# Kernel tuning notes

Measured on AMD Instinct MI355X. Metric: run time of the kernel, lower is better.

The kernel has to match this reference:

```python
import jax, jax.numpy as jnp
import numpy as np

B, N, D, A, E, T, H, O = 2, 2048, 64, 16, 2, 5, 128, 1


def setup_inputs() -> dict:
    key = jax.random.key(0)
    ks = jax.random.split(key, 12)
    s = 0.02  # torch init: normal(0, 0.02), biases zero
    return {
        "prop_state": jax.random.normal(ks[0], (B, N, D), jnp.float32),
        "annotation": jax.random.normal(ks[1], (B, N, A), jnp.float32),
        "adj_mat": jax.random.uniform(ks[2], (B, N, 2 * N * E), jnp.float32),
        "W_in": s * jax.random.normal(ks[3], (E, D, D), jnp.float32),
        "b_in": jnp.zeros((E, D), jnp.float32),
        "W_out": s * jax.random.normal(ks[4], (E, D, D), jnp.float32),
        "b_out": jnp.zeros((E, D), jnp.float32),
        "Wr": s * jax.random.normal(ks[5], (3 * D, D), jnp.float32),
        "br": jnp.zeros((D,), jnp.float32),
        "Wz": s * jax.random.normal(ks[6], (3 * D, D), jnp.float32),
        "bz": jnp.zeros((D,), jnp.float32),
        "Wh": s * jax.random.normal(ks[7], (3 * D, D), jnp.float32),
        "bh": jnp.zeros((D,), jnp.float32),
        "Wo1": s * jax.random.normal(ks[8], (D + A, H), jnp.float32),
        "bo1": jnp.zeros((H,), jnp.float32),
        "Wo2": s * jax.random.normal(ks[9], (H, O), jnp.float32),
        "bo2": jnp.zeros((O,), jnp.float32),
    }


def reference(prop_state, annotation, adj_mat, W_in, b_in, W_out, b_out,
              Wr, br, Wz, bz, Wh, bh, Wo1, bo1, Wo2, bo2):
    Bb, Nn, Dd = prop_state.shape
    Ee = W_in.shape[0]
    A_in = adj_mat[:, :, : Nn * Ee]   # [B, N, E*N]
    A_out = adj_mat[:, :, Nn * Ee :]  # [B, N, E*N]
    h = prop_state
    for _ in range(T):
        # per-edge-type linear maps; edge-type-major flatten (index = e*N + v)
        ins = (jnp.einsum('bnd,edk->benk', h, W_in) + b_in[None, :, None, :]).reshape(Bb, Ee * Nn, Dd)
        outs = (jnp.einsum('bnd,edk->benk', h, W_out) + b_out[None, :, None, :]).reshape(Bb, Ee * Nn, Dd)
        a_in = jnp.einsum('bnm,bmd->bnd', A_in, ins)
        a_out = jnp.einsum('bnm,bmd->bnd', A_out, outs)
        a = jnp.concatenate([a_in, a_out, h], axis=-1)          # [B, N, 3D]
        r = jax.nn.sigmoid(a @ Wr + br)
        z = jax.nn.sigmoid(a @ Wz + bz)
        joint = jnp.concatenate([a_in, a_out, r * h], axis=-1)  # [B, N, 3D]
        h_hat = jnp.tanh(joint @ Wh + bh)
        h = (1.0 - z) * h + z * h_hat
    x = jnp.concatenate([h, annotation], axis=-1)               # [B, N, D+A]
    x = jax.nn.sigmoid(x @ Wo1 + bo1)
    x = x @ Wo2 + bo2                                           # [B, N, O]
    return x.sum(axis=2)                                        # [B, N]
```

## Files before the change

### kernel.cpp

```cpp
#include <hip/hip_runtime.h>
#include <cstdint>
#include <cstddef>

#define B_ 2
#define N_ 2048
#define D_ 64
#define E_ 2
#define T_ 5

typedef short bf16x8 __attribute__((ext_vector_type(8)));
typedef unsigned short u16x8 __attribute__((ext_vector_type(8)));
typedef float f32x16 __attribute__((ext_vector_type(16)));

__device__ __forceinline__ unsigned short f2bf(float f) {
    unsigned int x = __float_as_uint(f);
    x += 0x7FFFu + ((x >> 16) & 1u);
    return (unsigned short)(x >> 16);
}

__global__ void convert_kernel(const float* __restrict__ adj, u16x8* __restrict__ Abf) {
    int rt = blockIdx.x, bd = blockIdx.y;
    int b = bd >> 1, dir = bd & 1;
    int tid = threadIdx.x;
    int lane = tid & 63;
    int row = rt * 32 + (lane & 31);
    int khalf = lane >> 5;
    const float* src = adj + ((size_t)(b * N_ + row)) * (2 * N_ * E_) + dir * (N_ * E_) + khalf * 8;
    u16x8* dst = Abf + ((size_t)(bd * 64 + rt) * 256) * 64 + lane;
    int kt0 = tid >> 6;
    #pragma unroll 4
    for (int i = 0; i < 64; ++i) {
        int kt = kt0 + 4 * i;
        const float* s = src + kt * 16;
        float4 f0 = *(const float4*)(s);
        float4 f1 = *(const float4*)(s + 4);
        u16x8 o;
        o[0] = f2bf(f0.x); o[1] = f2bf(f0.y); o[2] = f2bf(f0.z); o[3] = f2bf(f0.w);
        o[4] = f2bf(f1.x); o[5] = f2bf(f1.y); o[6] = f2bf(f1.z); o[7] = f2bf(f1.w);
        dst[(size_t)kt * 64] = o;
    }
}

__global__ void transform_kernel(const float* __restrict__ h,
                                 const float* __restrict__ W_in, const float* __restrict__ b_in,
                                 const float* __restrict__ W_out, const float* __restrict__ b_out,
                                 u16x8* __restrict__ VT) {
    int y = blockIdx.y;
    int e = y & 1, dir = (y >> 1) & 1, b = y >> 2;
    int bd = y >> 1;
    const float* W = (dir ? W_out : W_in) + e * D_ * D_;
    const float* bias = (dir ? b_out : b_in) + e * D_;
    int n0 = blockIdx.x * 64;

    __shared__ float hs[64][65];
    __shared__ float Ws[64][64];
    __shared__ float os[64][65];

    int tid = threadIdx.x;
    #pragma unroll
    for (int i = 0; i < 16; ++i) {
        int idx = tid + 256 * i;
        int r = idx >> 6, c = idx & 63;
        hs[r][c] = h[((size_t)(b * N_ + n0 + r)) * D_ + c];
        Ws[r][c] = W[idx];
    }
    __syncthreads();

    int g = tid >> 6, l = tid & 63;
    float acc[16];
    #pragma unroll
    for (int j = 0; j < 16; ++j) acc[j] = bias[g * 16 + j];
    for (int k = 0; k < 64; ++k) {
        float hv = hs[l][k];
        #pragma unroll
        for (int j = 0; j < 16; ++j) acc[j] = fmaf(hv, Ws[k][g * 16 + j], acc[j]);
    }
    #pragma unroll
    for (int j = 0; j < 16; ++j) os[l][g * 16 + j] = acc[j];
    __syncthreads();

    #pragma unroll
    for (int c = 0; c < 2; ++c) {
        int chunk = tid + 256 * c;
        int kt_local = chunk >> 7;
        int sub = (chunk >> 6) & 1;
        int ln = chunk & 63;
        int d = sub * 32 + (ln & 31);
        int nbase = kt_local * 16 + (ln >> 5) * 8;
        u16x8 o;
        #pragma unroll
        for (int j = 0; j < 8; ++j) o[j] = f2bf(os[nbase + j][d]);
        int ktg = e * 128 + blockIdx.x * 4 + kt_local;
        VT[((size_t)bd * 512 + ktg * 2 + sub) * 64 + ln] = o;
    }
}

__global__ void __launch_bounds__(512, 2) aggregate_kernel(
        const bf16x8* __restrict__ Abf, const bf16x8* __restrict__ VT,
        float* __restrict__ apart) {
    int bx = blockIdx.x;
    int bd = blockIdx.y;
    int sp = blockIdx.z;
    int tid = threadIdx.x;
    int w = tid >> 6, lane = tid & 63;
    int rt = bx * 8 + w;
    int kt0 = sp * 32;

    const bf16x8* Ap = Abf + ((size_t)(bd * 64 + rt) * 256 + kt0) * 64 + lane;
    const bf16x8* Vp = VT + (size_t)bd * 32768 + (size_t)kt0 * 128 + lane;

    f32x16 acc0 = {}, acc1 = {};
    #pragma unroll 4
    for (int kk = 0; kk < 32; ++kk) {
        bf16x8 a  = Ap[(size_t)kk * 64];
        bf16x8 b0 = Vp[(size_t)kk * 128];
        bf16x8 b1 = Vp[(size_t)kk * 128 + 64];
        acc0 = __builtin_amdgcn_mfma_f32_32x32x16_bf16(a, b0, acc0, 0, 0, 0);
        acc1 = __builtin_amdgcn_mfma_f32_32x32x16_bf16(a, b1, acc1, 0, 0, 0);
    }

    float* Cp = apart + ((size_t)(sp * 4 + bd) * 2048) * 64;
    int col = lane & 31;
    int rbase = rt * 32 + 4 * (lane >> 5);
    #pragma unroll
    for (int reg = 0; reg < 16; ++reg) {
        int row = rbase + (reg & 3) + 8 * (reg >> 2);
        Cp[(size_t)row * 64 + col]      = acc0[reg];
        Cp[(size_t)row * 64 + col + 32] = acc1[reg];
    }
}

__global__ void gru_kernel(float* __restrict__ h,
                           const float* __restrict__ apart,
                           const float* __restrict__ Wr, const float* __restrict__ br,
                           const float* __restrict__ Wz, const float* __restrict__ bz,
                           const float* __restrict__ Wh, const float* __restrict__ bh) {
    int tid = threadIdx.x;
    int grp = tid >> 6, d = tid & 63;
    int g = blockIdx.x * 16 + grp;
    int b = g >> 11, n = g & 2047;

    __shared__ float sa[16][3][64];
    float ain = 0.f, aout = 0.f;
    #pragma unroll
    for (int s = 0; s < 8; ++s) {
        ain  += apart[(((size_t)(s * 4 + b * 2    )) * 2048 + n) * 64 + d];
        aout += apart[(((size_t)(s * 4 + b * 2 + 1)) * 2048 + n) * 64 + d];
    }
    float h_d = h[(size_t)g * 64 + d];
    sa[grp][0][d] = ain;
    sa[grp][1][d] = aout;
    sa[grp][2][d] = h_d;
    __syncthreads();

    float accr = br[d], accz = bz[d];
    #pragma unroll 8
    for (int k = 0; k < 64; ++k) {
        float a0 = sa[grp][0][k], a1 = sa[grp][1][k], a2 = sa[grp][2][k];
        accr = fmaf(a0, Wr[k * 64 + d], accr);
        accr = fmaf(a1, Wr[(64 + k) * 64 + d], accr);
        accr = fmaf(a2, Wr[(128 + k) * 64 + d], accr);
        accz = fmaf(a0, Wz[k * 64 + d], accz);
        accz = fmaf(a1, Wz[(64 + k) * 64 + d], accz);
        accz = fmaf(a2, Wz[(128 + k) * 64 + d], accz);
    }
    float r = 1.0f / (1.0f + expf(-accr));
    float z = 1.0f / (1.0f + expf(-accz));

    __syncthreads();
    sa[grp][2][d] = r * h_d;
    __syncthreads();

    float acch = bh[d];
    #pragma unroll 8
    for (int k = 0; k < 64; ++k) {
        float a0 = sa[grp][0][k], a1 = sa[grp][1][k], a2 = sa[grp][2][k];
        acch = fmaf(a0, Wh[k * 64 + d], acch);
        acch = fmaf(a1, Wh[(64 + k) * 64 + d], acch);
        acch = fmaf(a2, Wh[(128 + k) * 64 + d], acch);
    }
    float hh = tanhf(acch);
    h[(size_t)g * 64 + d] = (1.0f - z) * h_d + z * hh;
}

__global__ void output_kernel(const float* __restrict__ h, const float* __restrict__ ann,
                              const float* __restrict__ Wo1, const float* __restrict__ bo1,
                              const float* __restrict__ Wo2, const float* __restrict__ bo2,
                              float* __restrict__ out) {
    int tid = threadIdx.x;
    int grp = tid >> 7, j = tid & 127;
    int g = blockIdx.x * 2 + grp;

    __shared__ float sx[2][80];
    __shared__ float sy[2][128];
    if (j < 64)       sx[grp][j] = h[(size_t)g * 64 + j];
    else if (j < 80)  sx[grp][j] = ann[(size_t)g * 16 + (j - 64)];
    __syncthreads();

    float acc = bo1[j];
    #pragma unroll
    for (int i = 0; i < 80; ++i) acc = fmaf(sx[grp][i], Wo1[i * 128 + j], acc);
    float y = 1.0f / (1.0f + expf(-acc));
    sy[grp][j] = y * Wo2[j];
    __syncthreads();

    if (j == 0) {
        float s = bo2[0];
        #pragma unroll
        for (int k = 0; k < 128; ++k) s += sy[grp][k];
        out[g] = s;
    }
}

extern "C" void kernel_launch(void* const* d_in, const int* in_sizes, int n_in,
                              void* d_out, int out_size, void* d_ws, size_t ws_size,
                              hipStream_t stream) {
    const float* prop = (const float*)d_in[0];
    const float* ann  = (const float*)d_in[1];
    const float* adj  = (const float*)d_in[2];
    const float* W_in = (const float*)d_in[3];
    const float* b_in = (const float*)d_in[4];
    const float* W_out= (const float*)d_in[5];
    const float* b_out= (const float*)d_in[6];
    const float* Wr   = (const float*)d_in[7];
    const float* br   = (const float*)d_in[8];
    const float* Wz   = (const float*)d_in[9];
    const float* bz   = (const float*)d_in[10];
    const float* Wh   = (const float*)d_in[11];
    const float* bh   = (const float*)d_in[12];
    const float* Wo1  = (const float*)d_in[13];
    const float* bo1  = (const float*)d_in[14];
    const float* Wo2  = (const float*)d_in[15];
    const float* bo2  = (const float*)d_in[16];
    float* out = (float*)d_out;

    char* ws = (char*)d_ws;
    u16x8* Abf   = (u16x8*)ws;
    u16x8* VT    = (u16x8*)(ws + (64ull << 20));
    float* apart = (float*)(ws + (66ull << 20));
    float* h     = (float*)(ws + (82ull << 20));

    convert_kernel<<<dim3(64, 4), 256, 0, stream>>>(adj, Abf);
    hipMemcpyAsync(h, prop, (size_t)B_ * N_ * D_ * sizeof(float),
                   hipMemcpyDeviceToDevice, stream);

    for (int t = 0; t < T_; ++t) {
        transform_kernel<<<dim3(32, 8), 256, 0, stream>>>(
            h, W_in, b_in, W_out, b_out, VT);
        aggregate_kernel<<<dim3(8, 4, 8), 512, 0, stream>>>(
            (const bf16x8*)Abf, (const bf16x8*)VT, apart);
        gru_kernel<<<dim3(B_ * N_ / 16), 1024, 0, stream>>>(
            h, apart, Wr, br, Wz, bz, Wh, bh);
    }
    output_kernel<<<dim3(B_ * N_ / 2), 256, 0, stream>>>(
        h, ann, Wo1, bo1, Wo2, bo2, out);
}
```

Before: 481.5 us.

## Stage adjacency fp32-to-bf16 conversion through LDS with coalesced row reads

The adjacency conversion kernel now reads each row's 512-column chunk with contiguous float4 loads across a warp, converts it to bf16 into shared memory, then writes the MFMA-tiled layout from shared memory. The grid is split along the column dimension as well, giving 8x more blocks for more memory-level parallelism. This targets the strided, poorly coalesced global reads of the original per-lane 32-byte accesses. The cost is an LDS round trip and a barrier per block.

Result: no change. 483.0 us (+0.3%).

```diff
diff --git a/kernel.cpp b/kernel.cpp
--- a/kernel.cpp
+++ b/kernel.cpp
@@ -19,25 +19,40 @@
 }
 
 __global__ void convert_kernel(const float* __restrict__ adj, u16x8* __restrict__ Abf) {
-    int rt = blockIdx.x, bd = blockIdx.y;
+    int rt = blockIdx.x, c = blockIdx.y, bd = blockIdx.z;
     int b = bd >> 1, dir = bd & 1;
     int tid = threadIdx.x;
-    int lane = tid & 63;
-    int row = rt * 32 + (lane & 31);
-    int khalf = lane >> 5;
-    const float* src = adj + ((size_t)(b * N_ + row)) * (2 * N_ * E_) + dir * (N_ * E_) + khalf * 8;
-    u16x8* dst = Abf + ((size_t)(bd * 64 + rt) * 256) * 64 + lane;
-    int kt0 = tid >> 6;
-    #pragma unroll 4
-    for (int i = 0; i < 64; ++i) {
-        int kt = kt0 + 4 * i;
-        const float* s = src + kt * 16;
-        float4 f0 = *(const float4*)(s);
-        float4 f1 = *(const float4*)(s + 4);
-        u16x8 o;
-        o[0] = f2bf(f0.x); o[1] = f2bf(f0.y); o[2] = f2bf(f0.z); o[3] = f2bf(f0.w);
-        o[4] = f2bf(f1.x); o[5] = f2bf(f1.y); o[6] = f2bf(f1.z); o[7] = f2bf(f1.w);
-        dst[(size_t)kt * 64] = o;
+
+    __shared__ __align__(16) unsigned short sb[32][520];
+
+    const float* base = adj + ((size_t)(b * N_ + rt * 32)) * (2 * N_ * E_) + dir * (N_ * E_) + c * 512;
+
+    #pragma unroll
+    for (int p = 0; p < 4; ++p) {
+        int r = p * 8 + (tid >> 5);
+        int i = tid & 31;
+        const float* rowp = base + (size_t)r * (2 * N_ * E_);
+        #pragma unroll
+        for (int j = 0; j < 4; ++j) {
+            float4 f = *(const float4*)(rowp + i * 4 + j * 128);
+            int kl = i * 4 + j * 128;
+            sb[r][kl + 0] = f2bf(f.x);
+            sb[r][kl + 1] = f2bf(f.y);
+            sb[r][kl + 2] = f2bf(f.z);
+            sb[r][kl + 3] = f2bf(f.w);
+        }
+    }
+    __syncthreads();
+
+    int l = tid & 63;
+    int row = l & 31, khalf = l >> 5;
+    int ktl0 = tid >> 6;
+    u16x8* dst = Abf + ((size_t)(bd * 64 + rt) * 256 + c * 32 + ktl0) * 64 + l;
+    #pragma unroll
+    for (int q = 0; q < 8; ++q) {
+        int ktl = ktl0 + q * 4;
+        u16x8 v = *(const u16x8*)&sb[row][ktl * 16 + khalf * 8];
+        dst[(size_t)q * 4 * 64] = v;
     }
 }
 
@@ -240,7 +255,7 @@
     float* apart = (float*)(ws + (66ull << 20));
     float* h     = (float*)(ws + (82ull << 20));
 
-    convert_kernel<<<dim3(64, 4), 256, 0, stream>>>(adj, Abf);
+    convert_kernel<<<dim3(64, 8, 4), 256, 0, stream>>>(adj, Abf);
     hipMemcpyAsync(h, prop, (size_t)B_ * N_ * D_ * sizeof(float),
                    hipMemcpyDeviceToDevice, stream);
 
```
